# Optimization experiments

Hardware: AMD Instinct MI355X
Metric: run time of the kernel (lower is better)

The kernel has to match this reference:

```python
import jax, jax.numpy as jnp
import numpy as np

N_NODES = 100000
N_EDGES = 1000000
IN_DIM = 64
OUT_DIM = 64


def graph_conv(src, dst, feat, W, b):
    # DGL GraphConv norm='none': sum incoming messages, then linear + bias
    msg = feat[src]                                        # [E, in_dim] gather
    agg = jax.ops.segment_sum(msg, dst, num_segments=N_NODES)  # [N, in_dim] scatter-add
    return agg @ W + b                                     # [N, out_dim]


def setup_inputs() -> dict:
    key = jax.random.key(0)
    ks = jax.random.split(key, 10)
    feat = jax.random.normal(ks[0], (N_NODES, IN_DIM), dtype=jnp.float32)
    shuf_feat = jax.random.normal(ks[1], (N_NODES, IN_DIM), dtype=jnp.float32)
    edge_src1 = jax.random.randint(ks[2], (N_EDGES,), 0, N_NODES, dtype=jnp.int32)
    edge_dst1 = jax.random.randint(ks[3], (N_EDGES,), 0, N_NODES, dtype=jnp.int32)
    edge_src2 = jax.random.randint(ks[4], (N_EDGES,), 0, N_NODES, dtype=jnp.int32)
    edge_dst2 = jax.random.randint(ks[5], (N_EDGES,), 0, N_NODES, dtype=jnp.int32)
    W1 = jax.random.normal(ks[6], (IN_DIM, OUT_DIM), dtype=jnp.float32) / np.sqrt(IN_DIM)
    b1 = jnp.zeros((OUT_DIM,), dtype=jnp.float32)
    W2 = jax.random.normal(ks[7], (IN_DIM, OUT_DIM), dtype=jnp.float32) / np.sqrt(IN_DIM)
    b2 = jnp.zeros((OUT_DIM,), dtype=jnp.float32)
    return {"feat": feat, "shuf_feat": shuf_feat,
            "edge_src1": edge_src1, "edge_dst1": edge_dst1,
            "edge_src2": edge_src2, "edge_dst2": edge_dst2,
            "W1": W1, "b1": b1, "W2": W2, "b2": b2}


def reference(feat, shuf_feat, edge_src1, edge_dst1, edge_src2, edge_dst2, W1, b1, W2, b2):
    h1 = graph_conv(edge_src1, edge_dst1, feat, W1, b1)        # encoder1 on graph
    h2 = graph_conv(edge_src2, edge_dst2, feat, W2, b2)        # encoder2 on dif_graph
    c1 = jax.nn.sigmoid(jnp.mean(h1, axis=0))                  # AvgPooling + sigmoid, [out_dim]
    c2 = jax.nn.sigmoid(jnp.mean(h2, axis=0))
    h3 = graph_conv(edge_src1, edge_dst1, shuf_feat, W1, b1)   # corrupted branch
    h4 = graph_conv(edge_src2, edge_dst2, shuf_feat, W2, b2)
    return (h1, h2, c1, c2, h3, h4)
```

## Files before the change

kernel.cpp:

```cpp
#include <hip/hip_runtime.h>
#include <hip/hip_bf16.h>

#define N_NODES 100000
#define N_EDGES 1000000
#define DIM 64

static const long long ND = (long long)N_NODES * DIM;

typedef float f4_t __attribute__((ext_vector_type(4)));
typedef unsigned u4_t __attribute__((ext_vector_type(4)));
typedef short s8_t __attribute__((ext_vector_type(8)));


#define NBUCK 98
#define BCAP 13312
#define OFFSTR 1028

#define WS_OFF1  200000
#define WS_OFF2  300744
#define WS_SORT1 401488
#define WS_SORT2 1706064
#define WS_CSUM  3010640
#define WS_BCUR  3010768
#define WS_WBT   3010964
#define WS_FBSB  3015060
#define WS_END   (WS_FBSB + 6400000)

#define CH_CONV 3125
#define CH_PARTG 489

__device__ __forceinline__ unsigned pk_bf16(float a, float b) {
    __hip_bfloat16 ha = __float2bfloat16(a), hb = __float2bfloat16(b);
    return (unsigned)(*(unsigned short*)&ha) | ((unsigned)(*(unsigned short*)&hb) << 16);
}
__device__ __forceinline__ float bf_lo(unsigned u) { return __uint_as_float(u << 16); }
__device__ __forceinline__ float bf_hi(unsigned u) { return __uint_as_float(u & 0xFFFF0000u); }

__global__ __launch_bounds__(256) void k_init(int* __restrict__ ws,
                                              const float* __restrict__ W1,
                                              const float* __restrict__ W2) {
    const int t = threadIdx.x;
    if (t < 128) ((float*)ws)[WS_CSUM + t] = 0.f;
    if (t < 196) ws[WS_BCUR + t] = 0;
    unsigned short* wbt = (unsigned short*)(ws + WS_WBT);
    for (int i = t; i < 8192; i += 256) {
        const int g = i >> 12, e = i & 4095;
        const int col = e >> 6, k = e & 63;
        const float* Wsrc = g ? W2 : W1;
        __hip_bfloat16 hb = __float2bfloat16(Wsrc[k * 64 + col]);
        wbt[i] = *(unsigned short*)&hb;
    }
}

__global__ __launch_bounds__(256) void k_convert_partition(
    const f4_t* __restrict__ feat4, const f4_t* __restrict__ shuf4,
    const int4* __restrict__ src1, const int4* __restrict__ dst1,
    const int4* __restrict__ src2, const int4* __restrict__ dst2,
    int* __restrict__ ws) {
    const int bid = blockIdx.x;
    const int t = threadIdx.x;
    if (bid < CH_CONV) {
        const long long NF4 = ND / 4;
        const long long base = ((long long)bid * 256 + t) * 4;
        uint2* T2 = (uint2*)(ws + WS_FBSB);
        #pragma unroll
        for (int k = 0; k < 4; ++k) {
            const long long j = base + k;
            if (j < NF4) {
                const f4_t v = __builtin_nontemporal_load(feat4 + j);
                const long long n = j >> 4, c = j & 15;
                T2[n * 32 + c] = make_uint2(pk_bf16(v.x, v.y), pk_bf16(v.z, v.w));
            } else if (j < 2 * NF4) {
                const long long jj = j - NF4;
                const f4_t v = __builtin_nontemporal_load(shuf4 + jj);
                const long long n = jj >> 4, c = jj & 15;
                T2[n * 32 + 16 + c] = make_uint2(pk_bf16(v.x, v.y), pk_bf16(v.z, v.w));
            }
        }
    } else {
        const int pid = bid - CH_CONV;
        const int g = pid >= CH_PARTG;
        const int px = g ? pid - CH_PARTG : pid;
        __shared__ int lcnt[NBUCK];
        __shared__ int lbase[NBUCK];
        const int4* sv4 = g ? src2 : src1;
        const int4* dv4 = g ? dst2 : dst1;
        int* sortp = ws + (g ? WS_SORT2 : WS_SORT1);
        int* bcur = ws + WS_BCUR + g * NBUCK;
        const int Q = N_EDGES / 4;

        const int q0 = px * 512 + t;
        const int q1 = q0 + 256;
        const bool v0 = q0 < Q, v1 = q1 < Q;
        int4 s0, d0, s1, d1;
        if (v0) { s0 = sv4[q0]; d0 = dv4[q0]; }
        if (v1) { s1 = sv4[q1]; d1 = dv4[q1]; }

        for (int i = t; i < NBUCK; i += 256) lcnt[i] = 0;
        __syncthreads();
        if (v0) {
            atomicAdd(&lcnt[d0.x >> 10], 1); atomicAdd(&lcnt[d0.y >> 10], 1);
            atomicAdd(&lcnt[d0.z >> 10], 1); atomicAdd(&lcnt[d0.w >> 10], 1);
        }
        if (v1) {
            atomicAdd(&lcnt[d1.x >> 10], 1); atomicAdd(&lcnt[d1.y >> 10], 1);
            atomicAdd(&lcnt[d1.z >> 10], 1); atomicAdd(&lcnt[d1.w >> 10], 1);
        }
        __syncthreads();
        if (t < NBUCK) lbase[t] = lcnt[t] ? t * BCAP + atomicAdd(&bcur[t], lcnt[t]) : 0;
        __syncthreads();

#define PUT(ss, dd) { const int b_ = (dd) >> 10; \
    const int pos_ = atomicAdd(&lbase[b_], 1); \
    sortp[pos_] = (ss) | (((dd) & 1023) << 17); }
        if (v0) { PUT(s0.x, d0.x); PUT(s0.y, d0.y); PUT(s0.z, d0.z); PUT(s0.w, d0.w); }
        if (v1) { PUT(s1.x, d1.x); PUT(s1.y, d1.y); PUT(s1.z, d1.z); PUT(s1.w, d1.w); }
#undef PUT
    }
}

__global__ __launch_bounds__(256) void k_place(int* __restrict__ ws) {
    const int g = blockIdx.y;
    const int b = blockIdx.x;
    const int t = threadIdx.x;
    __shared__ int pl[BCAP];
    __shared__ int lcur[1024];
    __shared__ int sscan[256];

    const int base = b * BCAP;
    int cnt = ws[WS_BCUR + g * NBUCK + b];
    if (cnt > BCAP) cnt = BCAP;
    int* sortp = ws + (g ? WS_SORT2 : WS_SORT1);
    int* off = ws + (g ? WS_OFF2 : WS_OFF1) + b * OFFSTR;

    for (int i = t; i < cnt; i += 256) pl[i] = sortp[base + i];
    for (int i = t; i < 1024; i += 256) lcur[i] = 0;
    __syncthreads();
    for (int i = t; i < cnt; i += 256) atomicAdd(&lcur[(pl[i] >> 17) & 1023], 1);
    __syncthreads();

    const int c0 = lcur[4 * t], c1 = lcur[4 * t + 1], c2 = lcur[4 * t + 2], c3 = lcur[4 * t + 3];
    sscan[t] = c0 + c1 + c2 + c3;
    __syncthreads();
    for (int d = 1; d < 256; d <<= 1) {
        int v = 0;
        if (t >= d) v = sscan[t - d];
        __syncthreads();
        sscan[t] += v;
        __syncthreads();
    }
    const int excl = (t == 0) ? 0 : sscan[t - 1];
    const int p0 = base + excl, p1 = p0 + c0, p2 = p1 + c1, p3 = p2 + c2;
    lcur[4 * t] = p0; lcur[4 * t + 1] = p1; lcur[4 * t + 2] = p2; lcur[4 * t + 3] = p3;
    *(int4*)(off + 4 * t) = make_int4(p0, p1, p2, p3);
    if (t == 255) off[1024] = base + cnt;
    __syncthreads();
    for (int i = t; i < cnt; i += 256) {
        const int p = pl[i];
        const int pos = atomicAdd(&lcur[(p >> 17) & 1023], 1);
        sortp[pos] = p & 0x1FFFF;
    }
}

#define ACC2(gv, sv) \
    ag[0] += bf_lo(gv.x); ag[1] += bf_hi(gv.x); \
    ag[2] += bf_lo(gv.y); ag[3] += bf_hi(gv.y); \
    ag[4] += bf_lo(gv.z); ag[5] += bf_hi(gv.z); \
    ag[6] += bf_lo(gv.w); ag[7] += bf_hi(gv.w); \
    as[0] += bf_lo(sv.x); as[1] += bf_hi(sv.x); \
    as[2] += bf_lo(sv.y); as[3] += bf_hi(sv.y); \
    as[4] += bf_lo(sv.z); as[5] += bf_hi(sv.z); \
    as[6] += bf_lo(sv.w); as[7] += bf_hi(sv.w);

__global__ __launch_bounds__(256) void k_gather(int* __restrict__ ws,
                                                float* __restrict__ out) {
    const int g = blockIdx.y;
    const int* offT   = ws + (g ? WS_OFF2 : WS_OFF1);
    const int* sorted = ws + (g ? WS_SORT2 : WS_SORT1);
    const uint4* T = (const uint4*)(ws + WS_FBSB);
    float* h_f = out + (g ? ND : 0);
    float* h_s = out + (g ? 3 * ND + 128 : 2 * ND + 128);

    const int t = threadIdx.x;
    const int wave = t >> 6;
    const int lane = t & 63;
    const int nslot = lane >> 3;
    const int sub = lane & 7;

    const int n = blockIdx.x * 32 + wave * 8 + nslot;
    if (n >= N_NODES) return;

    float ag[8] = {0.f, 0.f, 0.f, 0.f, 0.f, 0.f, 0.f, 0.f};
    float as[8] = {0.f, 0.f, 0.f, 0.f, 0.f, 0.f, 0.f, 0.f};

    const int* offb = offT + (n >> 10) * OFFSTR + (n & 1023);
    const int e0 = offb[0];
    const int e1 = offb[1];
    int e = e0;
    for (; e + 7 < e1; e += 8) {
        const int sA = sorted[e],     sB = sorted[e + 1];
        const int sC = sorted[e + 2], sD = sorted[e + 3];
        const int sE = sorted[e + 4], sF = sorted[e + 5];
        const int sG = sorted[e + 6], sH = sorted[e + 7];
        const uint4 gA = T[sA * 16 + sub], hA = T[sA * 16 + 8 + sub];
        const uint4 gB = T[sB * 16 + sub], hB = T[sB * 16 + 8 + sub];
        const uint4 gC = T[sC * 16 + sub], hC = T[sC * 16 + 8 + sub];
        const uint4 gD = T[sD * 16 + sub], hD = T[sD * 16 + 8 + sub];
        const uint4 gE = T[sE * 16 + sub], hE = T[sE * 16 + 8 + sub];
        const uint4 gF = T[sF * 16 + sub], hF = T[sF * 16 + 8 + sub];
        const uint4 gG = T[sG * 16 + sub], hG = T[sG * 16 + 8 + sub];
        const uint4 gH = T[sH * 16 + sub], hH = T[sH * 16 + 8 + sub];
        ACC2(gA, hA); ACC2(gB, hB); ACC2(gC, hC); ACC2(gD, hD);
        ACC2(gE, hE); ACC2(gF, hF); ACC2(gG, hG); ACC2(gH, hH);
    }
    for (; e + 3 < e1; e += 4) {
        const int sA = sorted[e],     sB = sorted[e + 1];
        const int sC = sorted[e + 2], sD = sorted[e + 3];
        const uint4 gA = T[sA * 16 + sub], hA = T[sA * 16 + 8 + sub];
        const uint4 gB = T[sB * 16 + sub], hB = T[sB * 16 + 8 + sub];
        const uint4 gC = T[sC * 16 + sub], hC = T[sC * 16 + 8 + sub];
        const uint4 gD = T[sD * 16 + sub], hD = T[sD * 16 + 8 + sub];
        ACC2(gA, hA); ACC2(gB, hB); ACC2(gC, hC); ACC2(gD, hD);
    }
    for (; e < e1; ++e) {
        const int s = sorted[e];
        const uint4 gv = T[s * 16 + sub], hv = T[s * 16 + 8 + sub];
        ACC2(gv, hv);
    }

    u4_t pf;
    pf.x = pk_bf16(ag[0], ag[1]); pf.y = pk_bf16(ag[2], ag[3]);
    pf.z = pk_bf16(ag[4], ag[5]); pf.w = pk_bf16(ag[6], ag[7]);
    __builtin_nontemporal_store(pf, (u4_t*)(h_f + (long long)n * DIM) + sub);
    u4_t ps;
    ps.x = pk_bf16(as[0], as[1]); ps.y = pk_bf16(as[2], as[3]);
    ps.z = pk_bf16(as[4], as[5]); ps.w = pk_bf16(as[6], as[7]);
    __builtin_nontemporal_store(ps, (u4_t*)(h_s + (long long)n * DIM) + sub);
}

__global__ __launch_bounds__(256) void k_htrans_mfma(int* __restrict__ ws,
                                                     const float* __restrict__ b1,
                                                     const float* __restrict__ b2,
                                                     float* __restrict__ out) {
    const int y = blockIdx.y;
    const int g = y & 1;
    float* hreg = out + (y == 0 ? 0 : y == 1 ? ND
                       : y == 2 ? 2 * ND + 128 : 3 * ND + 128);
    const float* bias = g ? b2 : b1;
    const s8_t* WT = (const s8_t*)((const unsigned short*)(ws + WS_WBT) + g * 4096);
    float* csum = (float*)ws + WS_CSUM + y * 64;

    __shared__ float red[4][64];

    const int t = threadIdx.x;
    const int wave = t >> 6;
    const int lane = t & 63;
    const int lm = lane & 15;
    const int lh = lane >> 4;

    s8_t bfr[4][2];
    #pragma unroll
    for (int nt = 0; nt < 4; ++nt) {
        bfr[nt][0] = WT[(nt * 16 + lm) * 8 + lh];
        bfr[nt][1] = WT[(nt * 16 + lm) * 8 + 4 + lh];
    }
    float bs[4];
    #pragma unroll
    for (int nt = 0; nt < 4; ++nt) bs[nt] = bias[nt * 16 + lm];

    float csloc[4] = {0.f, 0.f, 0.f, 0.f};
    const int r0base = blockIdx.x * 256 + wave * 64;

    #pragma unroll
    for (int tile = 0; tile < 4; ++tile) {
        const int r0 = r0base + tile * 16;
        const int rowA = r0 + lm;
        const int rA = rowA < N_NODES ? rowA : N_NODES - 1;
        const s8_t* arow = (const s8_t*)(hreg + (long long)rA * DIM);
        const s8_t a0 = arow[lh];
        const s8_t a1 = arow[4 + lh];

        f4_t acc[4];
        #pragma unroll
        for (int nt = 0; nt < 4; ++nt) {
            acc[nt] = (f4_t){0.f, 0.f, 0.f, 0.f};
            acc[nt] = __builtin_amdgcn_mfma_f32_16x16x32_bf16(a0, bfr[nt][0], acc[nt], 0, 0, 0);
            acc[nt] = __builtin_amdgcn_mfma_f32_16x16x32_bf16(a1, bfr[nt][1], acc[nt], 0, 0, 0);
        }
        #pragma unroll
        for (int nt = 0; nt < 4; ++nt) {
            #pragma unroll
            for (int i = 0; i < 4; ++i) {
                const int row = r0 + 4 * lh + i;
                if (row < N_NODES) {
                    const float v = acc[nt][i] + bs[nt];
                    hreg[(long long)row * DIM + nt * 16 + lm] = v;
                    csloc[nt] += v;
                }
            }
        }
    }

    if (y < 2) {
        #pragma unroll
        for (int nt = 0; nt < 4; ++nt) {
            csloc[nt] += __shfl_xor(csloc[nt], 16);
            csloc[nt] += __shfl_xor(csloc[nt], 32);
        }
        if (lane < 16) {
            #pragma unroll
            for (int nt = 0; nt < 4; ++nt) red[wave][nt * 16 + lane] = csloc[nt];
        }
        __syncthreads();
        if (t < 64) {
            const float s = red[0][t] + red[1][t] + red[2][t] + red[3][t];
            unsafeAtomicAdd(&csum[t], s);
        }
    }
}

__global__ void k_final(const float* __restrict__ ws_csum, float* __restrict__ out_c) {
    int t = threadIdx.x;
    float m = ws_csum[t] * (1.0f / (float)N_NODES);
    out_c[t] = 1.f / (1.f + expf(-m));
}

extern "C" void kernel_launch(void* const* d_in, const int* in_sizes, int n_in,
                              void* d_out, int out_size, void* d_ws, size_t ws_size,
                              hipStream_t stream) {
    const float* feat = (const float*)d_in[0];
    const float* shuf = (const float*)d_in[1];
    const int* src1 = (const int*)d_in[2];
    const int* dst1 = (const int*)d_in[3];
    const int* src2 = (const int*)d_in[4];
    const int* dst2 = (const int*)d_in[5];
    const float* W1 = (const float*)d_in[6];
    const float* b1 = (const float*)d_in[7];
    const float* W2 = (const float*)d_in[8];
    const float* b2 = (const float*)d_in[9];

    float* out = (float*)d_out;
    int* ws = (int*)d_ws;
    float* ws_f = (float*)d_ws;
    float* c_out = out + 2 * ND;

    k_init<<<1, 256, 0, stream>>>(ws, W1, W2);
    k_convert_partition<<<CH_CONV + 2 * CH_PARTG, 256, 0, stream>>>(
        (const f4_t*)feat, (const f4_t*)shuf,
        (const int4*)src1, (const int4*)dst1, (const int4*)src2, (const int4*)dst2, ws);
    k_place<<<dim3(NBUCK, 2), 256, 0, stream>>>(ws);
    k_gather<<<dim3((N_NODES + 31) / 32, 2), 256, 0, stream>>>(ws, out);
    k_htrans_mfma<<<dim3((N_NODES + 255) / 256, 4), 256, 0, stream>>>(ws, b1, b2, out);
    k_final<<<1, 128, 0, stream>>>(ws_f + WS_CSUM, c_out);
}
```

Before: 231.1 us.

## Fuse neighbor gather with MFMA linear transform via shared-memory staging

Merges the gather/aggregate kernel and the MFMA linear-transform kernel into one. Aggregated bf16 rows are staged in LDS, and each wave runs MFMA on a 16-row tile straight from shared memory. This removes the global round trip of the intermediate aggregates and one kernel launch. It adds a block-wide barrier after the gather phase, more LDS per block, and assumes N_NODES is divisible by 32 since bounds checks are removed.

After: 248.1 us. 7.4% more time.

```diff
diff --git a/kernel.cpp b/kernel.cpp
--- a/kernel.cpp
+++ b/kernel.cpp
@@ -172,14 +172,23 @@
     as[4] += bf_lo(sv.z); as[5] += bf_hi(sv.z); \
     as[6] += bf_lo(sv.w); as[7] += bf_hi(sv.w);
 
-__global__ __launch_bounds__(256) void k_gather(int* __restrict__ ws,
-                                                float* __restrict__ out) {
+__global__ __launch_bounds__(256) void k_gather_trans(int* __restrict__ ws,
+                                                      const float* __restrict__ b1,
+                                                      const float* __restrict__ b2,
+                                                      float* __restrict__ out) {
     const int g = blockIdx.y;
     const int* offT   = ws + (g ? WS_OFF2 : WS_OFF1);
     const int* sorted = ws + (g ? WS_SORT2 : WS_SORT1);
     const uint4* T = (const uint4*)(ws + WS_FBSB);
+    const float* bias = g ? b2 : b1;
+    const s8_t* WT = (const s8_t*)((const unsigned short*)(ws + WS_WBT) + g * 4096);
     float* h_f = out + (g ? ND : 0);
     float* h_s = out + (g ? 3 * ND + 128 : 2 * ND + 128);
+    float* csum = (float*)ws + WS_CSUM + g * 64;
+
+    __shared__ unsigned Af[32][36];
+    __shared__ unsigned As_[32][36];
+    __shared__ float red[2][64];
 
     const int t = threadIdx.x;
     const int wave = t >> 6;
@@ -187,8 +196,9 @@
     const int nslot = lane >> 3;
     const int sub = lane & 7;
 
-    const int n = blockIdx.x * 32 + wave * 8 + nslot;
-    if (n >= N_NODES) return;
+    const int n0 = blockIdx.x * 32;
+    const int lrow = wave * 8 + nslot;
+    const int n = n0 + lrow;
 
     float ag[8] = {0.f, 0.f, 0.f, 0.f, 0.f, 0.f, 0.f, 0.f};
     float as[8] = {0.f, 0.f, 0.f, 0.f, 0.f, 0.f, 0.f, 0.f};
@@ -231,30 +241,13 @@
     u4_t pf;
     pf.x = pk_bf16(ag[0], ag[1]); pf.y = pk_bf16(ag[2], ag[3]);
     pf.z = pk_bf16(ag[4], ag[5]); pf.w = pk_bf16(ag[6], ag[7]);
-    __builtin_nontemporal_store(pf, (u4_t*)(h_f + (long long)n * DIM) + sub);
+    *(u4_t*)&Af[lrow][sub * 4] = pf;
     u4_t ps;
     ps.x = pk_bf16(as[0], as[1]); ps.y = pk_bf16(as[2], as[3]);
     ps.z = pk_bf16(as[4], as[5]); ps.w = pk_bf16(as[6], as[7]);
-    __builtin_nontemporal_store(ps, (u4_t*)(h_s + (long long)n * DIM) + sub);
-}
-
-__global__ __launch_bounds__(256) void k_htrans_mfma(int* __restrict__ ws,
-                                                     const float* __restrict__ b1,
-                                                     const float* __restrict__ b2,
-                                                     float* __restrict__ out) {
-    const int y = blockIdx.y;
-    const int g = y & 1;
-    float* hreg = out + (y == 0 ? 0 : y == 1 ? ND
-                       : y == 2 ? 2 * ND + 128 : 3 * ND + 128);
-    const float* bias = g ? b2 : b1;
-    const s8_t* WT = (const s8_t*)((const unsigned short*)(ws + WS_WBT) + g * 4096);
-    float* csum = (float*)ws + WS_CSUM + y * 64;
-
-    __shared__ float red[4][64];
-
-    const int t = threadIdx.x;
-    const int wave = t >> 6;
-    const int lane = t & 63;
+    *(u4_t*)&As_[lrow][sub * 4] = ps;
+    __syncthreads();
+
     const int lm = lane & 15;
     const int lh = lane >> 4;
 
@@ -268,40 +261,35 @@
     #pragma unroll
     for (int nt = 0; nt < 4; ++nt) bs[nt] = bias[nt * 16 + lm];
 
+    const bool isf = wave < 2;
+    const int rbase = (wave & 1) * 16;
+    const unsigned (*A)[36] = isf ? Af : As_;
+    float* harr = isf ? h_f : h_s;
+
+    const s8_t a0 = *(const s8_t*)&A[rbase + lm][lh * 4];
+    const s8_t a1 = *(const s8_t*)&A[rbase + lm][16 + lh * 4];
+
+    f4_t acc[4];
+    #pragma unroll
+    for (int nt = 0; nt < 4; ++nt) {
+        acc[nt] = (f4_t){0.f, 0.f, 0.f, 0.f};
+        acc[nt] = __builtin_amdgcn_mfma_f32_16x16x32_bf16(a0, bfr[nt][0], acc[nt], 0, 0, 0);
+        acc[nt] = __builtin_amdgcn_mfma_f32_16x16x32_bf16(a1, bfr[nt][1], acc[nt], 0, 0, 0);
+    }
+
     float csloc[4] = {0.f, 0.f, 0.f, 0.f};
-    const int r0base = blockIdx.x * 256 + wave * 64;
-
     #pragma unroll
-    for (int tile = 0; tile < 4; ++tile) {
-        const int r0 = r0base + tile * 16;
-        const int rowA = r0 + lm;
-        const int rA = rowA < N_NODES ? rowA : N_NODES - 1;
-        const s8_t* arow = (const s8_t*)(hreg + (long long)rA * DIM);
-        const s8_t a0 = arow[lh];
-        const s8_t a1 = arow[4 + lh];
-
-        f4_t acc[4];
+    for (int nt = 0; nt < 4; ++nt) {
         #pragma unroll
-        for (int nt = 0; nt < 4; ++nt) {
-            acc[nt] = (f4_t){0.f, 0.f, 0.f, 0.f};
-            acc[nt] = __builtin_amdgcn_mfma_f32_16x16x32_bf16(a0, bfr[nt][0], acc[nt], 0, 0, 0);
-            acc[nt] = __builtin_amdgcn_mfma_f32_16x16x32_bf16(a1, bfr[nt][1], acc[nt], 0, 0, 0);
-        }
-        #pragma unroll
-        for (int nt = 0; nt < 4; ++nt) {
-            #pragma unroll
-            for (int i = 0; i < 4; ++i) {
-                const int row = r0 + 4 * lh + i;
-                if (row < N_NODES) {
-                    const float v = acc[nt][i] + bs[nt];
-                    hreg[(long long)row * DIM + nt * 16 + lm] = v;
-                    csloc[nt] += v;
-                }
-            }
-        }
-    }
-
-    if (y < 2) {
+        for (int i = 0; i < 4; ++i) {
+            const int row = rbase + 4 * lh + i;
+            const float v = acc[nt][i] + bs[nt];
+            harr[(long long)(n0 + row) * DIM + nt * 16 + lm] = v;
+            csloc[nt] += v;
+        }
+    }
+
+    if (isf) {
         #pragma unroll
         for (int nt = 0; nt < 4; ++nt) {
             csloc[nt] += __shfl_xor(csloc[nt], 16);
@@ -311,11 +299,11 @@
             #pragma unroll
             for (int nt = 0; nt < 4; ++nt) red[wave][nt * 16 + lane] = csloc[nt];
         }
-        __syncthreads();
-        if (t < 64) {
-            const float s = red[0][t] + red[1][t] + red[2][t] + red[3][t];
-            unsafeAtomicAdd(&csum[t], s);
-        }
+    }
+    __syncthreads();
+    if (t < 64) {
+        const float s = red[0][t] + red[1][t];
+        unsafeAtomicAdd(&csum[t], s);
     }
 }
 
@@ -349,7 +337,6 @@
         (const f4_t*)feat, (const f4_t*)shuf,
         (const int4*)src1, (const int4*)dst1, (const int4*)src2, (const int4*)dst2, ws);
     k_place<<<dim3(NBUCK, 2), 256, 0, stream>>>(ws);
-    k_gather<<<dim3((N_NODES + 31) / 32, 2), 256, 0, stream>>>(ws, out);
-    k_htrans_mfma<<<dim3((N_NODES + 255) / 256, 4), 256, 0, stream>>>(ws, b1, b2, out);
+    k_gather_trans<<<dim3(N_NODES / 32, 2), 256, 0, stream>>>(ws, b1, b2, out);
     k_final<<<1, 128, 0, stream>>>(ws_f + WS_CSUM, c_out);
 }
```
